# Kernel optimization log

Hardware: AMD Instinct MI355X
Metric: run time of the kernel (lower is better)

## Reference

```python
import jax, jax.numpy as jnp
import numpy as np

NUM_HEAD = 2
KR = 3          # kernel_range = [3, 3]
SHIFT = 1
N_P = KR * KR   # 9 taps
PAD = (KR // 2) * SHIFT  # 1
OFFSETS = [(i, j) for i in (-(KR // 2), 0, KR // 2) if True for j in ()]  # placeholder, real list below
OFFSETS = [(i, j) for i in range(-(KR // 2), KR // 2 + 1) for j in range(-(KR // 2), KR // 2 + 1)]


def _conv3x3(x, w, b):
    # x: [B,H,W,Cin], w: [3,3,Cin,Cout] -> SAME conv + bias
    y = jax.lax.conv_general_dilated(
        x, w, window_strides=(1, 1), padding='SAME',
        dimension_numbers=('NHWC', 'HWIO', 'NHWC'))
    return y + b


def setup_inputs() -> dict:
    key = jax.random.key(0)
    B, H, W, D = 4, 128, 128, 64
    ks = jax.random.split(key, 10)
    sc = 0.05  # small init like glorot
    return {
        'x': jax.random.normal(ks[0], (B, H, W, D), jnp.float32),
        # 1x1 conv kernels stored as matrices (equiv. to (1,1,Cin,Cout))
        'K_P': jax.random.normal(ks[1], (D, D * N_P), jnp.float32) * sc,
        'V_P': jax.random.normal(ks[2], (D, D * N_P), jnp.float32) * sc,
        'Q_P': jax.random.normal(ks[3], (D, D), jnp.float32) * sc,
        'ff1_kernel': jax.random.normal(ks[4], (D, D), jnp.float32) * sc,
        'ff1_bias': jax.random.normal(ks[5], (D,), jnp.float32) * sc,
        'ff2_kernel': jax.random.normal(ks[6], (3, 3, D, 2 * D), jnp.float32) * sc,
        'ff2_bias': jax.random.normal(ks[7], (2 * D,), jnp.float32) * sc,
        'ff3_kernel': jax.random.normal(ks[8], (3, 3, 2 * D, D), jnp.float32) * sc,
        'ff3_bias': jax.random.normal(ks[9], (D,), jnp.float32) * sc,
    }


def reference(x, K_P, V_P, Q_P, ff1_kernel, ff1_bias, ff2_kernel, ff2_bias,
              ff3_kernel, ff3_bias):
    B, H, W, D = x.shape
    hd = D // NUM_HEAD

    # 1x1 projections; K/V produce N_P channel chunks, one per tap
    x_k = jnp.einsum('bhwd,de->bhwe', x, K_P).reshape(B, H, W, N_P, D)
    x_v = jnp.einsum('bhwd,de->bhwe', x, V_P).reshape(B, H, W, N_P, D)
    x_q = jnp.einsum('bhwd,de->bhwe', x, Q_P)

    pad5 = ((0, 0), (PAD, PAD), (PAD, PAD), (0, 0), (0, 0))
    k_pad = jnp.pad(x_k, pad5)
    v_pad = jnp.pad(x_v, pad5)

    # tap t uses channel chunk t at spatial offset OFFSETS[t]*SHIFT
    def taps(padded):
        return jnp.stack(
            [padded[:, PAD + i * SHIFT:PAD + i * SHIFT + H,
                    PAD + j * SHIFT:PAD + j * SHIFT + W, t, :]
             for t, (i, j) in enumerate(OFFSETS)], axis=3)  # [B,H,W,N_P,D]

    k_taps = taps(k_pad)
    v_taps = taps(v_pad)

    # validity mask (padded taps get score 0 before softmax, as in original)
    m_pad = jnp.pad(jnp.ones((B, H, W), x.dtype), ((0, 0), (PAD, PAD), (PAD, PAD)))
    mask = jnp.stack(
        [m_pad[:, PAD + i * SHIFT:PAD + i * SHIFT + H,
               PAD + j * SHIFT:PAD + j * SHIFT + W]
         for (i, j) in OFFSETS], axis=3)  # [B,H,W,N_P]

    kh = k_taps.reshape(B, H, W, N_P, NUM_HEAD, hd)
    vh = v_taps.reshape(B, H, W, N_P, NUM_HEAD, hd)
    qh = x_q.reshape(B, H, W, NUM_HEAD, hd)

    # scores per head over taps; masked-multiply then /3, as in original
    scores = jnp.einsum('bhwtnc,bhwnc->bhwnt', kh, qh)
    scores = scores * mask[:, :, :, None, :] / 3.0
    alpha = jax.nn.softmax(scores, axis=-1)  # over taps
    attn = jnp.einsum('bhwnt,bhwtnc->bhwnc', alpha, vh).reshape(B, H, W, D)

    # FFN: 1x1 conv -> relu -> 3x3 conv -> relu -> 3x3 conv -> relu
    t = jax.nn.relu(jnp.einsum('bhwd,de->bhwe', attn, ff1_kernel) + ff1_bias)
    t = jax.nn.relu(_conv3x3(t, ff2_kernel, ff2_bias))
    t = jax.nn.relu(_conv3x3(t, ff3_kernel, ff3_bias))
    return t
```

## Files before the change

kernel.cpp:

```cpp
#include <hip/hip_runtime.h>


typedef _Float16 half8 __attribute__((ext_vector_type(8)));
typedef _Float16 half4v __attribute__((ext_vector_type(4)));
typedef float f32x4 __attribute__((ext_vector_type(4)));

__device__ __forceinline__ f32x4 mfma16(half8 a, half8 b, f32x4 c) {
  return __builtin_amdgcn_mfma_f32_16x16x32_f16(a, b, c, 0, 0, 0);
}
__device__ __forceinline__ half8 ldfrag(const _Float16* p) { return *(const half8*)p; }
__device__ __forceinline__ half8 zfrag() { half8 z = {}; return z; }

__device__ __forceinline__ void gload_lds16(const _Float16* g, _Float16* l) {
  __builtin_amdgcn_global_load_lds(
      (const __attribute__((address_space(1))) void*)g,
      (__attribute__((address_space(3))) void*)l, 16, 0, 0);
}
__device__ __forceinline__ void stage_frags(const _Float16* g, _Float16* l,
                                            int nfrag, int wid, int lane) {
#pragma unroll
  for (int c0 = 0; c0 < 4; ++c0) {
    int c = wid + c0 * 4;
    if (c < nfrag) gload_lds16(g + c * 512 + lane * 8, l + c * 512);
  }
}

__global__ __launch_bounds__(256) void cvt_x(const float* __restrict__ x,
                                             _Float16* __restrict__ xh) {
  int i = blockIdx.x * 256 + threadIdx.x;
  float4 v = ((const float4*)x)[i];
  half4v h = { (_Float16)v.x, (_Float16)v.y, (_Float16)v.z, (_Float16)v.w };
  *(half4v*)(xh + i * 4) = h;
}

__global__ __launch_bounds__(256) void repack(
    const float* __restrict__ Kp, const float* __restrict__ Vp,
    const float* __restrict__ Qp, const float* __restrict__ W1,
    const float* __restrict__ F2, const float* __restrict__ F3,
    _Float16* __restrict__ out) {
  int e = blockIdx.x * 256 + threadIdx.x;
  int j = e & 7, l = (e >> 3) & 63, f = e >> 9;
  int l15 = l & 15, q8 = (l >> 4) * 8;
  float v;
  if (f < 8)        { int mb = f >> 1, kb = f & 1;
                      v = Qp[(kb*32 + q8 + j) * 64 + mb*16 + l15]; }
  else if (f < 80)  { int g = f - 8, t = g >> 3, mb = (g >> 1) & 3, kb = g & 1;
                      v = Kp[(kb*32 + q8 + j) * 576 + t*64 + mb*16 + l15]; }
  else if (f < 152) { int g = f - 80, t = g >> 3, kb = (g >> 2) & 1, nb = g & 3;
                      v = Vp[(kb*32 + q8 + j) * 576 + t*64 + nb*16 + l15]; }
  else if (f < 160) { int g = f - 152, kb = g >> 2, nb = g & 3;
                      v = W1[(kb*32 + q8 + j) * 64 + nb*16 + l15]; }
  else if (f < 304) { int g = f - 160, t = g >> 4, kb = (g >> 3) & 1, nb = g & 7;
                      v = F2[(t*64 + kb*32 + q8 + j) * 128 + nb*16 + l15]; }
  else              { int g = f - 304, t = g >> 4, kb = (g >> 2) & 3, nb = g & 3;
                      v = F3[(t*128 + kb*32 + q8 + j) * 64 + nb*16 + l15]; }
  out[e] = (_Float16)v;
}

__global__ __launch_bounds__(256) void attn_ff1(
    const _Float16* __restrict__ xh, const _Float16* __restrict__ wf,
    const float* __restrict__ f1b, _Float16* __restrict__ t1g) {
  const int lane = threadIdx.x & 63, wid = threadIdx.x >> 6;
  const int l15 = lane & 15, q8 = (lane >> 4) * 8;
  const int row = blockIdx.x;
  const int p0 = row * 128 + wid * 32;
  const int h = row & 127;
  const int w0 = wid * 32;

  const _Float16* AQ = wf;
  const _Float16* AK = wf + 4096;
  const _Float16* BV = wf + 40960;
  const _Float16* B1 = wf + 77824;

  __shared__ _Float16 smem[9216];

  half8 ax0[2], ax1[2];
#pragma unroll
  for (int m = 0; m < 2; ++m) {
    const _Float16* xp = xh + (p0 + m * 16 + l15) * 64 + q8;
    ax0[m] = ldfrag(xp); ax1[m] = ldfrag(xp + 32);
  }

  f32x4 qT[2][4];
#pragma unroll
  for (int cb = 0; cb < 4; ++cb) {
    half8 aq0 = ldfrag(AQ + (cb * 2 + 0) * 512 + lane * 8);
    half8 aq1 = ldfrag(AQ + (cb * 2 + 1) * 512 + lane * 8);
#pragma unroll
    for (int m = 0; m < 2; ++m) {
      f32x4 c = {};
      c = mfma16(aq0, ax0[m], c);
      c = mfma16(aq1, ax1[m], c);
      qT[m][cb] = c;
    }
  }

  float sc[2][2][9];
#pragma unroll
  for (int m = 0; m < 2; ++m)
#pragma unroll
    for (int hd = 0; hd < 2; ++hd)
#pragma unroll
      for (int t = 0; t < 9; ++t) sc[m][hd][t] = 0.f;

  stage_frags(AK, smem, 8, wid, lane);
#pragma unroll
  for (int t = 0; t < 9; ++t) {
    _Float16* bw = smem + (t & 1) * 4096;
    __syncthreads();
    const int dh = t / 3 - 1, dw = t % 3 - 1;
    const bool rowok = (unsigned)(h + dh) < 128u;
    half8 sx0[2], sx1[2];
    if (rowok) {
#pragma unroll
      for (int m = 0; m < 2; ++m) {
        const bool cv = (unsigned)(w0 + m * 16 + l15 + dw) < 128u;
        const _Float16* sp = xh + (p0 + m * 16 + l15 + dh * 128 + dw) * 64 + q8;
        sx0[m] = cv ? ldfrag(sp) : zfrag();
        sx1[m] = cv ? ldfrag(sp + 32) : zfrag();
      }
    }
    if (t < 8) stage_frags(AK + (t + 1) * 4096, smem + ((t + 1) & 1) * 4096, 8, wid, lane);
    if (!rowok) continue;
    half8 kf[8];
#pragma unroll
    for (int f = 0; f < 8; ++f) kf[f] = ldfrag(bw + f * 512 + lane * 8);
#pragma unroll
    for (int m = 0; m < 2; ++m) {
      float pa = 0.f, pb = 0.f;
#pragma unroll
      for (int cb = 0; cb < 4; ++cb) {
        f32x4 c = {};
        c = mfma16(kf[cb * 2 + 0], sx0[m], c);
        c = mfma16(kf[cb * 2 + 1], sx1[m], c);
        float d = qT[m][cb].x * c.x + qT[m][cb].y * c.y
                + qT[m][cb].z * c.z + qT[m][cb].w * c.w;
        if (cb < 2) pa += d; else pb += d;
      }
      pa += __shfl_xor(pa, 16, 64); pa += __shfl_xor(pa, 32, 64);
      pb += __shfl_xor(pb, 16, 64); pb += __shfl_xor(pb, 32, 64);
      sc[m][0][t] = pa * (1.f / 3.f);
      sc[m][1][t] = pb * (1.f / 3.f);
    }
  }

#pragma unroll
  for (int m = 0; m < 2; ++m)
#pragma unroll
    for (int hd = 0; hd < 2; ++hd) {
      float mx = sc[m][hd][0];
#pragma unroll
      for (int t = 1; t < 9; ++t) mx = fmaxf(mx, sc[m][hd][t]);
      float s = 0.f;
#pragma unroll
      for (int t = 0; t < 9; ++t) { sc[m][hd][t] = __expf(sc[m][hd][t] - mx); s += sc[m][hd][t]; }
      s = 1.f / s;
#pragma unroll
      for (int t = 0; t < 9; ++t) sc[m][hd][t] *= s;
    }

  __syncthreads();
  stage_frags(BV, smem, 8, wid, lane);
  f32x4 at[2][4];
#pragma unroll
  for (int m = 0; m < 2; ++m)
#pragma unroll
    for (int nb = 0; nb < 4; ++nb) at[m][nb] = f32x4{};
#pragma unroll
  for (int t = 0; t < 9; ++t) {
    _Float16* bw = smem + (t & 1) * 4096;
    __syncthreads();
    const int dh = t / 3 - 1, dw = t % 3 - 1;
    const bool rowok = (unsigned)(h + dh) < 128u;
    half8 sx0[2], sx1[2];
    if (rowok) {
#pragma unroll
      for (int m = 0; m < 2; ++m) {
        const bool cv = (unsigned)(w0 + m * 16 + l15 + dw) < 128u;
        const _Float16* sp = xh + (p0 + m * 16 + l15 + dh * 128 + dw) * 64 + q8;
        sx0[m] = cv ? ldfrag(sp) : zfrag();
        sx1[m] = cv ? ldfrag(sp + 32) : zfrag();
      }
    }
    if (t < 8) stage_frags(BV + (t + 1) * 4096, smem + ((t + 1) & 1) * 4096, 8, wid, lane);
    if (!rowok) continue;
    half8 vf[8];
#pragma unroll
    for (int f = 0; f < 8; ++f) vf[f] = ldfrag(bw + f * 512 + lane * 8);
#pragma unroll
    for (int m = 0; m < 2; ++m) {
      _Float16 h0 = (_Float16)sc[m][0][t], h1 = (_Float16)sc[m][1][t];
      half8 b0 = {h0, h0, h0, h0, h0, h0, h0, h0};
      half8 b1 = {h1, h1, h1, h1, h1, h1, h1, h1};
      half8 s00 = sx0[m] * b0, s01 = sx1[m] * b0;
      half8 s10 = sx0[m] * b1, s11 = sx1[m] * b1;
#pragma unroll
      for (int nb = 0; nb < 2; ++nb) {
        at[m][nb]     = mfma16(s00, vf[0 * 4 + nb],     at[m][nb]);
        at[m][nb]     = mfma16(s01, vf[1 * 4 + nb],     at[m][nb]);
        at[m][nb + 2] = mfma16(s10, vf[0 * 4 + nb + 2], at[m][nb + 2]);
        at[m][nb + 2] = mfma16(s11, vf[1 * 4 + nb + 2], at[m][nb + 2]);
      }
    }
  }

  __syncthreads();
  _Float16* myt = smem + wid * 2304;
#pragma unroll
  for (int m = 0; m < 2; ++m)
#pragma unroll
    for (int nb = 0; nb < 4; ++nb)
#pragma unroll
      for (int r = 0; r < 4; ++r)
        myt[m * 1152 + ((lane >> 4) * 4 + r) * 72 + nb * 16 + l15] = (_Float16)at[m][nb][r];
#pragma unroll
  for (int m = 0; m < 2; ++m) {
    half8 aa0 = ldfrag(myt + m * 1152 + l15 * 72 + q8);
    half8 aa1 = ldfrag(myt + m * 1152 + l15 * 72 + 32 + q8);
#pragma unroll
    for (int nb = 0; nb < 4; ++nb) {
      f32x4 c = {};
      c = mfma16(aa0, ldfrag(B1 + (0 * 4 + nb) * 512 + lane * 8), c);
      c = mfma16(aa1, ldfrag(B1 + (1 * 4 + nb) * 512 + lane * 8), c);
      float bv = f1b[nb * 16 + l15];
#pragma unroll
      for (int r = 0; r < 4; ++r) {
        float v = fmaxf(c[r] + bv, 0.f);
        t1g[(p0 + m * 16 + (lane >> 4) * 4 + r) * 64 + nb * 16 + l15] = (_Float16)v;
      }
    }
  }
}

template <int KB, int NB>
__global__ __launch_bounds__(256) void conv3x3(
    const _Float16* __restrict__ in, const _Float16* __restrict__ wfrag,
    const float* __restrict__ bias, void* __restrict__ outp, int out_fp32) {
  const int lane = threadIdx.x & 63, wid = threadIdx.x >> 6;
  const int l15 = lane & 15, q8 = (lane >> 4) * 8;
  const int row = blockIdx.x;
  const int p0 = row * 128 + wid * 32;
  const int h = row & 127;
  const int w0 = wid * 32;
  const int CIN = KB * 32, COUT = NB * 16;

  __shared__ _Float16 smem[2 * 8192];

  f32x4 acc[2][NB];
#pragma unroll
  for (int m = 0; m < 2; ++m)
#pragma unroll
    for (int nb = 0; nb < NB; ++nb) acc[m][nb] = f32x4{};

  stage_frags(wfrag, smem, 16, wid, lane);
#pragma unroll
  for (int t = 0; t < 9; ++t) {
    _Float16* bw = smem + (t & 1) * 8192;
    __syncthreads();
    const int dh = t / 3 - 1, dw = t % 3 - 1;
    const bool rowok = (unsigned)(h + dh) < 128u;
    half8 a[2][KB];
    if (rowok) {
#pragma unroll
      for (int m = 0; m < 2; ++m) {
        const bool cv = (unsigned)(w0 + m * 16 + l15 + dw) < 128u;
        const _Float16* sp = in + (p0 + m * 16 + l15 + dh * 128 + dw) * CIN + q8;
#pragma unroll
        for (int kb = 0; kb < KB; ++kb) a[m][kb] = cv ? ldfrag(sp + kb * 32) : zfrag();
      }
    }
    if (t < 8) stage_frags(wfrag + (t + 1) * 8192, smem + ((t + 1) & 1) * 8192, 16, wid, lane);
    if (!rowok) continue;
#pragma unroll
    for (int nb = 0; nb < NB; ++nb) {
#pragma unroll
      for (int kb = 0; kb < KB; ++kb) {
        half8 b = ldfrag(bw + (kb * NB + nb) * 512 + lane * 8);
        acc[0][nb] = mfma16(a[0][kb], b, acc[0][nb]);
        acc[1][nb] = mfma16(a[1][kb], b, acc[1][nb]);
      }
    }
  }

#pragma unroll
  for (int m = 0; m < 2; ++m)
#pragma unroll
    for (int nb = 0; nb < NB; ++nb) {
      float bv = bias[nb * 16 + l15];
#pragma unroll
      for (int r = 0; r < 4; ++r) {
        float v = fmaxf(acc[m][nb][r] + bv, 0.f);
        int idx = (p0 + m * 16 + (lane >> 4) * 4 + r) * COUT + nb * 16 + l15;
        if (out_fp32) ((float*)outp)[idx] = v;
        else          ((_Float16*)outp)[idx] = (_Float16)v;
      }
    }
}

extern "C" void kernel_launch(void* const* d_in, const int* in_sizes, int n_in,
                              void* d_out, int out_size, void* d_ws, size_t ws_size,
                              hipStream_t stream) {
  (void)in_sizes; (void)n_in; (void)out_size; (void)ws_size;
  const float* x   = (const float*)d_in[0];
  const float* Kp  = (const float*)d_in[1];
  const float* Vp  = (const float*)d_in[2];
  const float* Qp  = (const float*)d_in[3];
  const float* f1w = (const float*)d_in[4];
  const float* f1b = (const float*)d_in[5];
  const float* f2w = (const float*)d_in[6];
  const float* f2b = (const float*)d_in[7];
  const float* f3w = (const float*)d_in[8];
  const float* f3b = (const float*)d_in[9];

  _Float16* xh  = (_Float16*)d_ws;
  _Float16* wf  = xh + 4194304;
  _Float16* t2g = wf + 229376;
  _Float16* t1g = (_Float16*)d_out;

  cvt_x<<<4096, 256, 0, stream>>>(x, xh);
  repack<<<896, 256, 0, stream>>>(Kp, Vp, Qp, f1w, f2w, f3w, wf);
  attn_ff1<<<512, 256, 0, stream>>>(xh, wf, f1b, t1g);
  conv3x3<2, 8><<<512, 256, 0, stream>>>(t1g, wf + 81920, f2b, t2g, 0);
  conv3x3<4, 4><<<512, 256, 0, stream>>>(t2g, wf + 155648, f3b, d_out, 1);
}
```

Measured before the change: 162.4 us.

## Stage all tap weights into LDS once and prefetch next-tap activations

The attention+FF1 kernel and both 3x3 conv kernels now copy their full weight sets into large dynamic shared memory up front, instead of double-buffering one tap at a time. This removes the per-tap __syncthreads barriers. Activation fragments for the next tap are prefetched into registers while the current tap computes. The cost is up to about 150KB of LDS per block, which limits each CU to one resident block with four waves. That leaves less room to hide latency and serialises the 512 blocks into more waves; each block also copies the whole weight set from L2 before it can start.

Measured after the change: 170.8 us. 5.2% more time.

```diff
diff --git a/kernel.cpp b/kernel.cpp
--- a/kernel.cpp
+++ b/kernel.cpp
@@ -16,13 +16,13 @@
       (const __attribute__((address_space(1))) void*)g,
       (__attribute__((address_space(3))) void*)l, 16, 0, 0);
 }
-__device__ __forceinline__ void stage_frags(const _Float16* g, _Float16* l,
-                                            int nfrag, int wid, int lane) {
-#pragma unroll
-  for (int c0 = 0; c0 < 4; ++c0) {
-    int c = wid + c0 * 4;
-    if (c < nfrag) gload_lds16(g + c * 512 + lane * 8, l + c * 512);
-  }
+__device__ __forceinline__ void stage_all(const _Float16* g, _Float16* l,
+                                          int nfrag, int wid, int lane) {
+  const int per = nfrag >> 2;
+  const _Float16* gw = g + (size_t)(wid * per) * 512;
+  _Float16* lw = l + wid * per * 512;
+  for (int i = 0; i < per; ++i)
+    gload_lds16(gw + i * 512 + lane * 8, lw + i * 512);
 }
 
 __global__ __launch_bounds__(256) void cvt_x(const float* __restrict__ x,
@@ -57,9 +57,10 @@
   out[e] = (_Float16)v;
 }
 
-__global__ __launch_bounds__(256) void attn_ff1(
+__global__ __launch_bounds__(256, 1) void attn_ff1(
     const _Float16* __restrict__ xh, const _Float16* __restrict__ wf,
     const float* __restrict__ f1b, _Float16* __restrict__ t1g) {
+  extern __shared__ _Float16 smem[];
   const int lane = threadIdx.x & 63, wid = threadIdx.x >> 6;
   const int l15 = lane & 15, q8 = (lane >> 4) * 8;
   const int row = blockIdx.x;
@@ -67,25 +68,19 @@
   const int h = row & 127;
   const int w0 = wid * 32;
 
-  const _Float16* AQ = wf;
-  const _Float16* AK = wf + 4096;
-  const _Float16* BV = wf + 40960;
-  const _Float16* B1 = wf + 77824;
-
-  __shared__ _Float16 smem[9216];
+  stage_all(wf + 4096, smem, 152, wid, lane);
 
   half8 ax0[2], ax1[2];
 #pragma unroll
   for (int m = 0; m < 2; ++m) {
-    const _Float16* xp = xh + (p0 + m * 16 + l15) * 64 + q8;
+    const _Float16* xp = xh + (size_t)(p0 + m * 16 + l15) * 64 + q8;
     ax0[m] = ldfrag(xp); ax1[m] = ldfrag(xp + 32);
   }
-
   f32x4 qT[2][4];
 #pragma unroll
   for (int cb = 0; cb < 4; ++cb) {
-    half8 aq0 = ldfrag(AQ + (cb * 2 + 0) * 512 + lane * 8);
-    half8 aq1 = ldfrag(AQ + (cb * 2 + 1) * 512 + lane * 8);
+    half8 aq0 = ldfrag(wf + (cb * 2 + 0) * 512 + lane * 8);
+    half8 aq1 = ldfrag(wf + (cb * 2 + 1) * 512 + lane * 8);
 #pragma unroll
     for (int m = 0; m < 2; ++m) {
       f32x4 c = {};
@@ -95,52 +90,64 @@
     }
   }
 
+  __syncthreads();
+
   float sc[2][2][9];
-#pragma unroll
-  for (int m = 0; m < 2; ++m)
-#pragma unroll
-    for (int hd = 0; hd < 2; ++hd)
-#pragma unroll
-      for (int t = 0; t < 9; ++t) sc[m][hd][t] = 0.f;
-
-  stage_frags(AK, smem, 8, wid, lane);
+  half8 sx0[2], sx1[2];
+  {
+    const bool rk = (unsigned)(h - 1) < 128u;
+#pragma unroll
+    for (int m = 0; m < 2; ++m) {
+      const bool cv = rk && ((unsigned)(w0 + m * 16 + l15 - 1) < 128u);
+      const _Float16* sp = xh + (size_t)(p0 + m * 16 + l15 - 129) * 64 + q8;
+      sx0[m] = cv ? ldfrag(sp) : zfrag();
+      sx1[m] = cv ? ldfrag(sp + 32) : zfrag();
+    }
+  }
 #pragma unroll
   for (int t = 0; t < 9; ++t) {
-    _Float16* bw = smem + (t & 1) * 4096;
-    __syncthreads();
     const int dh = t / 3 - 1, dw = t % 3 - 1;
     const bool rowok = (unsigned)(h + dh) < 128u;
-    half8 sx0[2], sx1[2];
+    half8 nx0[2], nx1[2];
+    if (t < 8) {
+      const int dh2 = (t + 1) / 3 - 1, dw2 = (t + 1) % 3 - 1;
+      const bool rk2 = (unsigned)(h + dh2) < 128u;
+#pragma unroll
+      for (int m = 0; m < 2; ++m) {
+        const bool cv = rk2 && ((unsigned)(w0 + m * 16 + l15 + dw2) < 128u);
+        const _Float16* sp = xh + (size_t)(p0 + m * 16 + l15 + dh2 * 128 + dw2) * 64 + q8;
+        nx0[m] = cv ? ldfrag(sp) : zfrag();
+        nx1[m] = cv ? ldfrag(sp + 32) : zfrag();
+      }
+    }
     if (rowok) {
-#pragma unroll
-      for (int m = 0; m < 2; ++m) {
-        const bool cv = (unsigned)(w0 + m * 16 + l15 + dw) < 128u;
-        const _Float16* sp = xh + (p0 + m * 16 + l15 + dh * 128 + dw) * 64 + q8;
-        sx0[m] = cv ? ldfrag(sp) : zfrag();
-        sx1[m] = cv ? ldfrag(sp + 32) : zfrag();
-      }
-    }
-    if (t < 8) stage_frags(AK + (t + 1) * 4096, smem + ((t + 1) & 1) * 4096, 8, wid, lane);
-    if (!rowok) continue;
-    half8 kf[8];
-#pragma unroll
-    for (int f = 0; f < 8; ++f) kf[f] = ldfrag(bw + f * 512 + lane * 8);
-#pragma unroll
-    for (int m = 0; m < 2; ++m) {
-      float pa = 0.f, pb = 0.f;
-#pragma unroll
-      for (int cb = 0; cb < 4; ++cb) {
-        f32x4 c = {};
-        c = mfma16(kf[cb * 2 + 0], sx0[m], c);
-        c = mfma16(kf[cb * 2 + 1], sx1[m], c);
-        float d = qT[m][cb].x * c.x + qT[m][cb].y * c.y
-                + qT[m][cb].z * c.z + qT[m][cb].w * c.w;
-        if (cb < 2) pa += d; else pb += d;
-      }
-      pa += __shfl_xor(pa, 16, 64); pa += __shfl_xor(pa, 32, 64);
-      pb += __shfl_xor(pb, 16, 64); pb += __shfl_xor(pb, 32, 64);
-      sc[m][0][t] = pa * (1.f / 3.f);
-      sc[m][1][t] = pb * (1.f / 3.f);
+      half8 kf[8];
+#pragma unroll
+      for (int f = 0; f < 8; ++f) kf[f] = ldfrag(smem + (t * 8 + f) * 512 + lane * 8);
+#pragma unroll
+      for (int m = 0; m < 2; ++m) {
+        float pa = 0.f, pb = 0.f;
+#pragma unroll
+        for (int cb = 0; cb < 4; ++cb) {
+          f32x4 c = {};
+          c = mfma16(kf[cb * 2 + 0], sx0[m], c);
+          c = mfma16(kf[cb * 2 + 1], sx1[m], c);
+          float d = qT[m][cb].x * c.x + qT[m][cb].y * c.y
+                  + qT[m][cb].z * c.z + qT[m][cb].w * c.w;
+          if (cb < 2) pa += d; else pb += d;
+        }
+        pa += __shfl_xor(pa, 16, 64); pa += __shfl_xor(pa, 32, 64);
+        pb += __shfl_xor(pb, 16, 64); pb += __shfl_xor(pb, 32, 64);
+        sc[m][0][t] = pa * (1.f / 3.f);
+        sc[m][1][t] = pb * (1.f / 3.f);
+      }
+    } else {
+#pragma unroll
+      for (int m = 0; m < 2; ++m) { sc[m][0][t] = 0.f; sc[m][1][t] = 0.f; }
+    }
+    if (t < 8) {
+#pragma unroll
+      for (int m = 0; m < 2; ++m) { sx0[m] = nx0[m]; sx1[m] = nx1[m]; }
     }
   }
 
@@ -159,48 +166,61 @@
       for (int t = 0; t < 9; ++t) sc[m][hd][t] *= s;
     }
 
-  __syncthreads();
-  stage_frags(BV, smem, 8, wid, lane);
+  const _Float16* BVl = smem + 36864;
   f32x4 at[2][4];
 #pragma unroll
   for (int m = 0; m < 2; ++m)
 #pragma unroll
     for (int nb = 0; nb < 4; ++nb) at[m][nb] = f32x4{};
+  {
+    const bool rk = (unsigned)(h - 1) < 128u;
+#pragma unroll
+    for (int m = 0; m < 2; ++m) {
+      const bool cv = rk && ((unsigned)(w0 + m * 16 + l15 - 1) < 128u);
+      const _Float16* sp = xh + (size_t)(p0 + m * 16 + l15 - 129) * 64 + q8;
+      sx0[m] = cv ? ldfrag(sp) : zfrag();
+      sx1[m] = cv ? ldfrag(sp + 32) : zfrag();
+    }
+  }
 #pragma unroll
   for (int t = 0; t < 9; ++t) {
-    _Float16* bw = smem + (t & 1) * 4096;
-    __syncthreads();
-    const int dh = t / 3 - 1, dw = t % 3 - 1;
+    const int dh = t / 3 - 1;
     const bool rowok = (unsigned)(h + dh) < 128u;
-    half8 sx0[2], sx1[2];
+    half8 nx0[2], nx1[2];
+    if (t < 8) {
+      const int dh2 = (t + 1) / 3 - 1, dw2 = (t + 1) % 3 - 1;
+      const bool rk2 = (unsigned)(h + dh2) < 128u;
+#pragma unroll
+      for (int m = 0; m < 2; ++m) {
+        const bool cv = rk2 && ((unsigned)(w0 + m * 16 + l15 + dw2) < 128u);
+        const _Float16* sp = xh + (size_t)(p0 + m * 16 + l15 + dh2 * 128 + dw2) * 64 + q8;
+        nx0[m] = cv ? ldfrag(sp) : zfrag();
+        nx1[m] = cv ? ldfrag(sp + 32) : zfrag();
+      }
+    }
     if (rowok) {
-#pragma unroll
-      for (int m = 0; m < 2; ++m) {
-        const bool cv = (unsigned)(w0 + m * 16 + l15 + dw) < 128u;
-        const _Float16* sp = xh + (p0 + m * 16 + l15 + dh * 128 + dw) * 64 + q8;
-        sx0[m] = cv ? ldfrag(sp) : zfrag();
-        sx1[m] = cv ? ldfrag(sp + 32) : zfrag();
-      }
-    }
-    if (t < 8) stage_frags(BV + (t + 1) * 4096, smem + ((t + 1) & 1) * 4096, 8, wid, lane);
-    if (!rowok) continue;
-    half8 vf[8];
-#pragma unroll
-    for (int f = 0; f < 8; ++f) vf[f] = ldfrag(bw + f * 512 + lane * 8);
-#pragma unroll
-    for (int m = 0; m < 2; ++m) {
-      _Float16 h0 = (_Float16)sc[m][0][t], h1 = (_Float16)sc[m][1][t];
-      half8 b0 = {h0, h0, h0, h0, h0, h0, h0, h0};
-      half8 b1 = {h1, h1, h1, h1, h1, h1, h1, h1};
-      half8 s00 = sx0[m] * b0, s01 = sx1[m] * b0;
-      half8 s10 = sx0[m] * b1, s11 = sx1[m] * b1;
-#pragma unroll
-      for (int nb = 0; nb < 2; ++nb) {
-        at[m][nb]     = mfma16(s00, vf[0 * 4 + nb],     at[m][nb]);
-        at[m][nb]     = mfma16(s01, vf[1 * 4 + nb],     at[m][nb]);
-        at[m][nb + 2] = mfma16(s10, vf[0 * 4 + nb + 2], at[m][nb + 2]);
-        at[m][nb + 2] = mfma16(s11, vf[1 * 4 + nb + 2], at[m][nb + 2]);
-      }
+      half8 vf[8];
+#pragma unroll
+      for (int f = 0; f < 8; ++f) vf[f] = ldfrag(BVl + (t * 8 + f) * 512 + lane * 8);
+#pragma unroll
+      for (int m = 0; m < 2; ++m) {
+        _Float16 h0 = (_Float16)sc[m][0][t], h1 = (_Float16)sc[m][1][t];
+        half8 b0 = {h0, h0, h0, h0, h0, h0, h0, h0};
+        half8 b1 = {h1, h1, h1, h1, h1, h1, h1, h1};
+        half8 s00 = sx0[m] * b0, s01 = sx1[m] * b0;
+        half8 s10 = sx0[m] * b1, s11 = sx1[m] * b1;
+#pragma unroll
+        for (int nb = 0; nb < 2; ++nb) {
+          at[m][nb]     = mfma16(s00, vf[0 * 4 + nb],     at[m][nb]);
+          at[m][nb]     = mfma16(s01, vf[1 * 4 + nb],     at[m][nb]);
+          at[m][nb + 2] = mfma16(s10, vf[0 * 4 + nb + 2], at[m][nb + 2]);
+          at[m][nb + 2] = mfma16(s11, vf[1 * 4 + nb + 2], at[m][nb + 2]);
+        }
+      }
+    }
+    if (t < 8) {
+#pragma unroll
+      for (int m = 0; m < 2; ++m) { sx0[m] = nx0[m]; sx1[m] = nx1[m]; }
     }
   }
 
@@ -213,6 +233,7 @@
 #pragma unroll
       for (int r = 0; r < 4; ++r)
         myt[m * 1152 + ((lane >> 4) * 4 + r) * 72 + nb * 16 + l15] = (_Float16)at[m][nb][r];
+  const _Float16* B1l = smem + 73728;
 #pragma unroll
   for (int m = 0; m < 2; ++m) {
     half8 aa0 = ldfrag(myt + m * 1152 + l15 * 72 + q8);
@@ -220,22 +241,23 @@
 #pragma unroll
     for (int nb = 0; nb < 4; ++nb) {
       f32x4 c = {};
-      c = mfma16(aa0, ldfrag(B1 + (0 * 4 + nb) * 512 + lane * 8), c);
-      c = mfma16(aa1, ldfrag(B1 + (1 * 4 + nb) * 512 + lane * 8), c);
+      c = mfma16(aa0, ldfrag(B1l + (0 * 4 + nb) * 512 + lane * 8), c);
+      c = mfma16(aa1, ldfrag(B1l + (1 * 4 + nb) * 512 + lane * 8), c);
       float bv = f1b[nb * 16 + l15];
 #pragma unroll
       for (int r = 0; r < 4; ++r) {
         float v = fmaxf(c[r] + bv, 0.f);
-        t1g[(p0 + m * 16 + (lane >> 4) * 4 + r) * 64 + nb * 16 + l15] = (_Float16)v;
+        t1g[(size_t)(p0 + m * 16 + (lane >> 4) * 4 + r) * 64 + nb * 16 + l15] = (_Float16)v;
       }
     }
   }
 }
 
 template <int KB, int NB>
-__global__ __launch_bounds__(256) void conv3x3(
+__global__ __launch_bounds__(256, 1) void conv3x3(
     const _Float16* __restrict__ in, const _Float16* __restrict__ wfrag,
     const float* __restrict__ bias, void* __restrict__ outp, int out_fp32) {
+  extern __shared__ _Float16 smem[];
   const int lane = threadIdx.x & 63, wid = threadIdx.x >> 6;
   const int l15 = lane & 15, q8 = (lane >> 4) * 8;
   const int row = blockIdx.x;
@@ -244,7 +266,7 @@
   const int w0 = wid * 32;
   const int CIN = KB * 32, COUT = NB * 16;
 
-  __shared__ _Float16 smem[2 * 8192];
+  stage_all(wfrag, smem, 9 * KB * NB, wid, lane);
 
   f32x4 acc[2][NB];
 #pragma unroll
@@ -252,33 +274,51 @@
 #pragma unroll
     for (int nb = 0; nb < NB; ++nb) acc[m][nb] = f32x4{};
 
-  stage_frags(wfrag, smem, 16, wid, lane);
+  __syncthreads();
+
+  half8 a[2][KB];
+  {
+    const bool rk = (unsigned)(h - 1) < 128u;
+#pragma unroll
+    for (int m = 0; m < 2; ++m) {
+      const bool cv = rk && ((unsigned)(w0 + m * 16 + l15 - 1) < 128u);
+      const _Float16* sp = in + (size_t)(p0 + m * 16 + l15 - 129) * CIN + q8;
+#pragma unroll
+      for (int kb = 0; kb < KB; ++kb) a[m][kb] = cv ? ldfrag(sp + kb * 32) : zfrag();
+    }
+  }
 #pragma unroll
   for (int t = 0; t < 9; ++t) {
-    _Float16* bw = smem + (t & 1) * 8192;
-    __syncthreads();
-    const int dh = t / 3 - 1, dw = t % 3 - 1;
+    const int dh = t / 3 - 1;
     const bool rowok = (unsigned)(h + dh) < 128u;
-    half8 a[2][KB];
+    half8 an[2][KB];
+    if (t < 8) {
+      const int dh2 = (t + 1) / 3 - 1, dw2 = (t + 1) % 3 - 1;
+      const bool rk2 = (unsigned)(h + dh2) < 128u;
+#pragma unroll
+      for (int m = 0; m < 2; ++m) {
+        const bool cv = rk2 && ((unsigned)(w0 + m * 16 + l15 + dw2) < 128u);
+        const _Float16* sp = in + (size_t)(p0 + m * 16 + l15 + dh2 * 128 + dw2) * CIN + q8;
+#pragma unroll
+        for (int kb = 0; kb < KB; ++kb) an[m][kb] = cv ? ldfrag(sp + kb * 32) : zfrag();
+      }
+    }
     if (rowok) {
 #pragma unroll
-      for (int m = 0; m < 2; ++m) {
-        const bool cv = (unsigned)(w0 + m * 16 + l15 + dw) < 128u;
-        const _Float16* sp = in + (p0 + m * 16 + l15 + dh * 128 + dw) * CIN + q8;
-#pragma unroll
-        for (int kb = 0; kb < KB; ++kb) a[m][kb] = cv ? ldfrag(sp + kb * 32) : zfrag();
-      }
-    }
-    if (t < 8) stage_frags(wfrag + (t + 1) * 8192, smem + ((t + 1) & 1) * 8192, 16, wid, lane);
-    if (!rowok) continue;
-#pragma unroll
-    for (int nb = 0; nb < NB; ++nb) {
-#pragma unroll
-      for (int kb = 0; kb < KB; ++kb) {
-        half8 b = ldfrag(bw + (kb * NB + nb) * 512 + lane * 8);
-        acc[0][nb] = mfma16(a[0][kb], b, acc[0][nb]);
-        acc[1][nb] = mfma16(a[1][kb], b, acc[1][nb]);
-      }
+      for (int nb = 0; nb < NB; ++nb) {
+#pragma unroll
+        for (int kb = 0; kb < KB; ++kb) {
+          half8 b = ldfrag(smem + ((t * KB + kb) * NB + nb) * 512 + lane * 8);
+          acc[0][nb] = mfma16(a[0][kb], b, acc[0][nb]);
+          acc[1][nb] = mfma16(a[1][kb], b, acc[1][nb]);
+        }
+      }
+    }
+    if (t < 8) {
+#pragma unroll
+      for (int m = 0; m < 2; ++m)
+#pragma unroll
+        for (int kb = 0; kb < KB; ++kb) a[m][kb] = an[m][kb];
     }
   }
 
@@ -290,7 +330,7 @@
 #pragma unroll
       for (int r = 0; r < 4; ++r) {
         float v = fmaxf(acc[m][nb][r] + bv, 0.f);
-        int idx = (p0 + m * 16 + (lane >> 4) * 4 + r) * COUT + nb * 16 + l15;
+        size_t idx = (size_t)(p0 + m * 16 + (lane >> 4) * 4 + r) * COUT + nb * 16 + l15;
         if (out_fp32) ((float*)outp)[idx] = v;
         else          ((_Float16*)outp)[idx] = (_Float16)v;
       }
@@ -317,9 +357,16 @@
   _Float16* t2g = wf + 229376;
   _Float16* t1g = (_Float16*)d_out;
 
+  (void)hipFuncSetAttribute((const void*)attn_ff1,
+      hipFuncAttributeMaxDynamicSharedMemorySize, 155648);
+  (void)hipFuncSetAttribute((const void*)conv3x3<2, 8>,
+      hipFuncAttributeMaxDynamicSharedMemorySize, 147456);
+  (void)hipFuncSetAttribute((const void*)conv3x3<4, 4>,
+      hipFuncAttributeMaxDynamicSharedMemorySize, 147456);
+
   cvt_x<<<4096, 256, 0, stream>>>(x, xh);
   repack<<<896, 256, 0, stream>>>(Kp, Vp, Qp, f1w, f2w, f3w, wf);
-  attn_ff1<<<512, 256, 0, stream>>>(xh, wf, f1b, t1g);
-  conv3x3<2, 8><<<512, 256, 0, stream>>>(t1g, wf + 81920, f2b, t2g, 0);
-  conv3x3<4, 4><<<512, 256, 0, stream>>>(t2g, wf + 155648, f3b, d_out, 1);
-}
+  attn_ff1<<<512, 256, 155648, stream>>>(xh, wf, f1b, t1g);
+  conv3x3<2, 8><<<512, 256, 147456, stream>>>(t1g, wf + 81920, f2b, t2g, 0);
+  conv3x3<4, 4><<<512, 256, 147456, stream>>>(t2g, wf + 155648, f3b, d_out, 1);
+}
```
